# Kernel optimization log

Measured on AMD Instinct MI355X. Metric: run time of the kernel, lower is better.

## Reference

```python
import jax, jax.numpy as jnp
from jax import lax
import numpy as np

MARKER_NUM = 50000
E = 256          # embed_dim
D = 512          # d_model
K = 16           # sample_size / neighbor_num
B = 128
S = 128
BETA = 0.1
MAX_TIME = 1000.0


def setup_inputs() -> dict:
    key = jax.random.key(0)
    ks = jax.random.split(key, 12)
    def lin(k, fan_in, shape):
        return (jax.random.normal(k, shape, jnp.float32) / np.sqrt(fan_in)).astype(jnp.float32)
    return {
        "marker_data": jax.random.randint(ks[0], (B, S), 0, MARKER_NUM),
        "time_data": jax.random.uniform(ks[1], (B, S), jnp.float32),
        "mask_data": jnp.ones((B, S), jnp.float32),
        "embedding": jax.random.normal(ks[2], (MARKER_NUM, E), jnp.float32) * 0.05,
        "neighbor_list": jax.random.randint(ks[3], (MARKER_NUM, K), 0, MARKER_NUM),
        "neighbor_prob": jax.random.uniform(ks[4], (MARKER_NUM, K), jnp.float32),
        "W_te": lin(ks[5], 1, (1, E)), "b_te": jnp.zeros((E,), jnp.float32),
        "W_el": lin(ks[6], E, (E, D)), "b_el": jnp.zeros((D,), jnp.float32),
        "W_ih": lin(ks[7], D, (D, D)), "b_ih": jnp.zeros((D,), jnp.float32),
        "W_hh": lin(ks[8], D, (D, D)), "b_hh": jnp.zeros((D,), jnp.float32),
        "W_time": lin(ks[9], D, (D, 1)), "b_time": jnp.zeros((1,), jnp.float32),
        "W_mk": lin(ks[10], E + D, (E + D, 1)), "b_mk": jnp.zeros((1,), jnp.float32),
    }


def reference(marker_data, time_data, mask_data, embedding, neighbor_list, neighbor_prob,
              W_te, b_te, W_el, b_el, W_ih, b_ih, W_hh, b_hh, W_time, b_time, W_mk, b_mk):
    leaky = lambda x: jnp.where(x >= 0, x, 0.01 * x)  # LeakyReLU(0.01)
    Bn, Sn = marker_data.shape
    L = 1 + (Sn - 1) * (K - 1)  # final candidate_list / prob_list width
    R = 1 + (Sn - 1) * K        # final neighbor_prob_record width

    cand0 = jnp.zeros((Bn, L), jnp.int32).at[:, 0].set(marker_data[:, 0].astype(jnp.int32))
    prob0 = jnp.zeros((Bn, L), jnp.float32).at[:, 0].set(1.0)  # zero pad -> never sampled
    nrec0 = jnp.ones((Bn, R), jnp.float32)
    chosen0 = jnp.zeros((Bn, 1), jnp.int32)
    h0 = jnp.zeros((Bn, D), jnp.float32)
    carry0 = (h0, time_data[:, 0:1], marker_data[:, 0:1].astype(jnp.int32), cand0, prob0, nrec0, chosen0)
    keys = jax.random.split(jax.random.key(42), Sn - 1)

    def step(carry, xt):
        t, key = xt
        h, last_t, last_m, cand, prob, nrec, chosen = carry
        # embedding of (marker, time)
        time_emb = last_t @ W_te + b_te                       # (B,E)
        vec = embedding[last_m[:, 0]] + BETA * time_emb       # (B,E)
        x = leaky(vec @ W_el + b_el)                          # (B,D)
        # single-layer tanh RNN step (nn.RNN)
        h = jnp.tanh(x @ W_ih + b_ih + h @ W_hh + b_hh)
        new_t = last_t + jax.nn.softplus(h @ W_time + b_time)  # (B,1)
        new_mask = (new_t < MAX_TIME).astype(jnp.float32)
        # sampled neighbors of last marker
        neigh = neighbor_list[last_m[:, 0]].astype(jnp.int32)  # (B,K)
        p_neigh = neighbor_prob[last_m[:, 0]]                  # (B,K)
        nrec = lax.dynamic_update_slice(nrec, p_neigh, (0, 1 + t * K))
        inf = jnp.concatenate([embedding[neigh], jnp.broadcast_to(h[:, None, :], (Bn, K, D))], axis=-1)
        mprob = jax.nn.softmax((inf @ W_mk + b_mk)[..., 0], axis=1)  # (B,K)
        cand = lax.dynamic_update_slice(cand, neigh[:, 1:], (0, 1 + t * (K - 1)))
        chosen_p = jnp.take_along_axis(prob, chosen, 1)        # (B,1)
        attached = chosen_p * mprob                            # (B,K)
        prob = prob.at[jnp.arange(Bn), chosen[:, 0]].set(attached[:, 0])
        prob = lax.dynamic_update_slice(prob, attached[:, 1:], (0, 1 + t * (K - 1)))
        # torch.multinomial(prob_list, 1) == categorical over normalized probs
        logits = jnp.where(prob > 0, jnp.log(jnp.maximum(prob, 1e-38)), -1e30)
        new_chosen = jax.random.categorical(key, lax.stop_gradient(logits), axis=1)[:, None].astype(jnp.int32)
        new_m = jnp.take_along_axis(cand, new_chosen, 1)       # (B,1)
        sel_np = jnp.take_along_axis(nrec, new_chosen, 1)
        sel_sp = jnp.take_along_axis(prob, new_chosen, 1)
        new_carry = (h, new_t, new_m, cand, prob, nrec, new_chosen)
        return new_carry, (new_m[:, 0], new_t[:, 0], new_mask[:, 0], sel_np[:, 0], sel_sp[:, 0])

    _, (ms, ts, mk, nps, sps) = lax.scan(step, carry0, (jnp.arange(Sn - 1), keys))
    ones = jnp.ones((Bn, 1), jnp.float32)
    marker_res = jnp.concatenate([marker_data[:, 0:1].astype(jnp.int32), ms.T], axis=1)
    time_res = jnp.concatenate([time_data[:, 0:1], ts.T], axis=1)
    mask_res = jnp.concatenate([mask_data[:, 0:1], mk.T], axis=1)
    total_neighbor_prob = jnp.concatenate([ones, nps.T], axis=1)
    total_sample_prob = jnp.concatenate([ones, sps.T], axis=1)
    return (marker_res, time_res, mask_res, total_neighbor_prob, total_sample_prob)
```

## Files before the change

### kernel.cpp

```cpp
#include <hip/hip_runtime.h>
#include <stdint.h>
#include <stddef.h>

#define BB 128
#define SS 128
#define EE 256
#define DD 512
#define KK 16
#define LL 1906
#define RR 2033
#define NSTEP 127

static __device__ __forceinline__ uint32_t rotl32(uint32_t v, int r) {
  return (v << r) | (v >> (32 - r));
}

static __device__ __forceinline__ void tf2x32(uint32_t k0, uint32_t k1,
                                              uint32_t x0, uint32_t x1,
                                              uint32_t &o0, uint32_t &o1) {
  uint32_t ks2 = k0 ^ k1 ^ 0x1BD11BDAu;
  x0 += k0; x1 += k1;
#define TFR(r) { x0 += x1; x1 = rotl32(x1, (r)); x1 ^= x0; }
  TFR(13) TFR(15) TFR(26) TFR(6)
  x0 += k1;  x1 += ks2 + 1u;
  TFR(17) TFR(29) TFR(16) TFR(24)
  x0 += ks2; x1 += k0 + 2u;
  TFR(13) TFR(15) TFR(26) TFR(6)
  x0 += k0;  x1 += k1 + 3u;
  TFR(17) TFR(29) TFR(16) TFR(24)
  x0 += k1;  x1 += ks2 + 4u;
  TFR(13) TFR(15) TFR(26) TFR(6)
  x0 += ks2; x1 += k0 + 5u;
#undef TFR
  o0 = x0; o1 = x1;
}

static __device__ __forceinline__ float jax_gumbel(uint32_t bits) {
  float f = __uint_as_float((bits >> 9) | 0x3F800000u) - 1.0f;
  float u = fmaxf(f, 1.17549435e-38f);
  return -logf(-logf(u));
}

__global__ __launch_bounds__(1024, 4) void rnn_gen_kernel(
    const int*   __restrict__ marker_data,
    const float* __restrict__ time_data,
    const float* __restrict__ mask_data,
    const float* __restrict__ embedding,
    const int*   __restrict__ neighbor_list,
    const float* __restrict__ neighbor_prob,
    const float* __restrict__ W_te,
    const float* __restrict__ b_te,
    const float* __restrict__ W_el,
    const float* __restrict__ b_el,
    const float* __restrict__ W_ih,
    const float* __restrict__ b_ih,
    const float* __restrict__ W_hh,
    const float* __restrict__ b_hh,
    const float* __restrict__ W_time,
    const float* __restrict__ b_time,
    const float* __restrict__ W_mk,
    const float* __restrict__ b_mk,
    float* __restrict__ out)
{
  __shared__ double s_pd[8][DD];
  __shared__ double s_pd2[8][DD];
  __shared__ double s_edot[KK];
  __shared__ double s_rt[8];
  __shared__ double s_rm[8];
  __shared__ float  s_prob[LL];
  __shared__ int    s_cand[LL];
  __shared__ float  s_nrec[RR];
  __shared__ float  s_x[DD];
  __shared__ float  s_h[DD];
  __shared__ float  s_vec[EE];
  __shared__ float  s_red_z[16];
  __shared__ int    s_red_i[16];
  __shared__ int    s_neigh[KK];
  __shared__ float  s_last_t;
  __shared__ int    s_last_m;
  __shared__ int    s_chosen;
  __shared__ float  s_newt;
  __shared__ uint32_t s_k0, s_k1;

  const int b   = blockIdx.x;
  const int tid = threadIdx.x;

  for (int i = tid; i < LL; i += 1024) { s_prob[i] = 0.0f; s_cand[i] = 0; }
  for (int i = tid; i < RR; i += 1024) s_nrec[i] = 1.0f;
  if (tid < DD) s_h[tid] = 0.0f;
  if (tid == 0) {
    int   m0 = marker_data[b * SS];
    float t0 = time_data[b * SS];
    s_cand[0] = m0; s_prob[0] = 1.0f;
    s_last_m = m0; s_last_t = t0; s_chosen = 0;
    out[0 * BB * SS + b * SS + 0] = (float)m0;
    out[1 * BB * SS + b * SS + 0] = t0;
    out[2 * BB * SS + b * SS + 0] = mask_data[b * SS];
    out[3 * BB * SS + b * SS + 0] = 1.0f;
    out[4 * BB * SS + b * SS + 0] = 1.0f;
  }
  __syncthreads();

  for (int t = 0; t < NSTEP; ++t) {
    const int   m  = s_last_m;
    const float lt = s_last_t;

    if (tid == 768) {
      uint32_t o0, o1;
      tf2x32(0u, 42u, 0u, (uint32_t)t, o0, o1);
      s_k0 = o0; s_k1 = o1;
    }
    if (tid < EE) {
      float te = __fadd_rn(__fmul_rn(lt, W_te[tid]), b_te[tid]);
      s_vec[tid] = __fadd_rn(embedding[(size_t)m * EE + tid], __fmul_rn(0.1f, te));
    }
    if (tid >= 256 && tid < 256 + KK) {
      int k = tid - 256;
      int nb = neighbor_list[(size_t)m * KK + k];
      s_neigh[k] = nb;
      s_nrec[1 + t * KK + k] = neighbor_prob[(size_t)m * KK + k];
      if (k >= 1) s_cand[1 + t * (KK - 1) + (k - 1)] = nb;
    }
    __syncthreads();

    float4 ev0 = make_float4(0.f,0.f,0.f,0.f), ev1 = ev0;
    if (tid >= 512) {
      int k = (tid - 512) >> 5, l32 = tid & 31;
      const float4* er = (const float4*)(embedding + (size_t)s_neigh[k] * EE);
      ev0 = er[2 * l32]; ev1 = er[2 * l32 + 1];
    }
    const int jg = tid & 127;
    const int sl = tid >> 7;
    {
      const int i0 = sl << 5;
      const float4* W4 = (const float4*)W_el + (size_t)i0 * 128 + jg;
      double d0 = 0.0, d1 = 0.0, d2 = 0.0, d3 = 0.0;
#pragma unroll 4
      for (int i = 0; i < 32; i += 4) {
        float4 a4 = *(const float4*)&s_vec[i0 + i];
        float4 w0 = W4[0], w1 = W4[128], w2 = W4[256], w3 = W4[384];
        W4 += 512;
        d0 = fma((double)a4.x, (double)w0.x, d0); d1 = fma((double)a4.x, (double)w0.y, d1);
        d2 = fma((double)a4.x, (double)w0.z, d2); d3 = fma((double)a4.x, (double)w0.w, d3);
        d0 = fma((double)a4.y, (double)w1.x, d0); d1 = fma((double)a4.y, (double)w1.y, d1);
        d2 = fma((double)a4.y, (double)w1.z, d2); d3 = fma((double)a4.y, (double)w1.w, d3);
        d0 = fma((double)a4.z, (double)w2.x, d0); d1 = fma((double)a4.z, (double)w2.y, d1);
        d2 = fma((double)a4.z, (double)w2.z, d2); d3 = fma((double)a4.z, (double)w2.w, d3);
        d0 = fma((double)a4.w, (double)w3.x, d0); d1 = fma((double)a4.w, (double)w3.y, d1);
        d2 = fma((double)a4.w, (double)w3.z, d2); d3 = fma((double)a4.w, (double)w3.w, d3);
      }
      double* pd = &s_pd[sl][4 * jg];
      pd[0] = d0; pd[1] = d1; pd[2] = d2; pd[3] = d3;
    }
    {
      const int i0 = sl << 6;
      const float4* W4 = (const float4*)W_hh + (size_t)i0 * 128 + jg;
      double d0 = 0.0, d1 = 0.0, d2 = 0.0, d3 = 0.0;
#pragma unroll 4
      for (int i = 0; i < 64; i += 4) {
        float4 a4 = *(const float4*)&s_h[i0 + i];
        float4 w0 = W4[0], w1 = W4[128], w2 = W4[256], w3 = W4[384];
        W4 += 512;
        d0 = fma((double)a4.x, (double)w0.x, d0); d1 = fma((double)a4.x, (double)w0.y, d1);
        d2 = fma((double)a4.x, (double)w0.z, d2); d3 = fma((double)a4.x, (double)w0.w, d3);
        d0 = fma((double)a4.y, (double)w1.x, d0); d1 = fma((double)a4.y, (double)w1.y, d1);
        d2 = fma((double)a4.y, (double)w1.z, d2); d3 = fma((double)a4.y, (double)w1.w, d3);
        d0 = fma((double)a4.z, (double)w2.x, d0); d1 = fma((double)a4.z, (double)w2.y, d1);
        d2 = fma((double)a4.z, (double)w2.z, d2); d3 = fma((double)a4.z, (double)w2.w, d3);
        d0 = fma((double)a4.w, (double)w3.x, d0); d1 = fma((double)a4.w, (double)w3.y, d1);
        d2 = fma((double)a4.w, (double)w3.z, d2); d3 = fma((double)a4.w, (double)w3.w, d3);
      }
      double* pd = &s_pd2[sl][4 * jg];
      pd[0] = d0; pd[1] = d1; pd[2] = d2; pd[3] = d3;
    }
    __syncthreads();

    if (tid < DD) {
      double d = ((s_pd[0][tid] + s_pd[1][tid]) + (s_pd[2][tid] + s_pd[3][tid]))
               + ((s_pd[4][tid] + s_pd[5][tid]) + (s_pd[6][tid] + s_pd[7][tid]));
      float z = __fadd_rn((float)d, b_el[tid]);
      s_x[tid] = (z >= 0.0f) ? z : __fmul_rn(0.01f, z);
    }
    __syncthreads();

    {
      const int i0 = sl << 6;
      const float4* W4 = (const float4*)W_ih + (size_t)i0 * 128 + jg;
      double d0 = 0.0, d1 = 0.0, d2 = 0.0, d3 = 0.0;
#pragma unroll 4
      for (int i = 0; i < 64; i += 4) {
        float4 a4 = *(const float4*)&s_x[i0 + i];
        float4 w0 = W4[0], w1 = W4[128], w2 = W4[256], w3 = W4[384];
        W4 += 512;
        d0 = fma((double)a4.x, (double)w0.x, d0); d1 = fma((double)a4.x, (double)w0.y, d1);
        d2 = fma((double)a4.x, (double)w0.z, d2); d3 = fma((double)a4.x, (double)w0.w, d3);
        d0 = fma((double)a4.y, (double)w1.x, d0); d1 = fma((double)a4.y, (double)w1.y, d1);
        d2 = fma((double)a4.y, (double)w1.z, d2); d3 = fma((double)a4.y, (double)w1.w, d3);
        d0 = fma((double)a4.z, (double)w2.x, d0); d1 = fma((double)a4.z, (double)w2.y, d1);
        d2 = fma((double)a4.z, (double)w2.z, d2); d3 = fma((double)a4.z, (double)w2.w, d3);
        d0 = fma((double)a4.w, (double)w3.x, d0); d1 = fma((double)a4.w, (double)w3.y, d1);
        d2 = fma((double)a4.w, (double)w3.z, d2); d3 = fma((double)a4.w, (double)w3.w, d3);
      }
      double* pd = &s_pd[sl][4 * jg];
      pd[0] = d0; pd[1] = d1; pd[2] = d2; pd[3] = d3;
    }
    __syncthreads();

    if (tid < DD) {
      double ih = ((s_pd[0][tid] + s_pd[1][tid]) + (s_pd[2][tid] + s_pd[3][tid]))
                + ((s_pd[4][tid] + s_pd[5][tid]) + (s_pd[6][tid] + s_pd[7][tid]));
      double hh = ((s_pd2[0][tid] + s_pd2[1][tid]) + (s_pd2[2][tid] + s_pd2[3][tid]))
                + ((s_pd2[4][tid] + s_pd2[5][tid]) + (s_pd2[6][tid] + s_pd2[7][tid]));
      float p = __fadd_rn(__fadd_rn(__fadd_rn((float)ih, b_ih[tid]), (float)hh), b_hh[tid]);
      float hf = (float)tanh((double)p);
      s_h[tid] = hf;
      double hv = (double)hf;
      double pt = hv * (double)W_time[tid];
      double pm = hv * (double)W_mk[EE + tid];
      for (int off = 32; off > 0; off >>= 1) {
        pt += __shfl_down(pt, off);
        pm += __shfl_down(pm, off);
      }
      if ((tid & 63) == 0) { s_rt[tid >> 6] = pt; s_rm[tid >> 6] = pm; }
    } else {
      int k = (tid - 512) >> 5, l32 = tid & 31;
      const float4* wm4 = (const float4*)W_mk;
      float4 wm0 = wm4[2 * l32], wm1 = wm4[2 * l32 + 1];
      double acc = 0.0;
      acc = fma((double)ev0.x, (double)wm0.x, acc);
      acc = fma((double)ev0.y, (double)wm0.y, acc);
      acc = fma((double)ev0.z, (double)wm0.z, acc);
      acc = fma((double)ev0.w, (double)wm0.w, acc);
      acc = fma((double)ev1.x, (double)wm1.x, acc);
      acc = fma((double)ev1.y, (double)wm1.y, acc);
      acc = fma((double)ev1.z, (double)wm1.z, acc);
      acc = fma((double)ev1.w, (double)wm1.w, acc);
      for (int off = 16; off > 0; off >>= 1) acc += __shfl_down(acc, off, 32);
      if (l32 == 0) s_edot[k] = acc;
    }
    __syncthreads();

    if (tid < KK) {
      double hmk = ((s_rm[0] + s_rm[1]) + (s_rm[2] + s_rm[3]))
                 + ((s_rm[4] + s_rm[5]) + (s_rm[6] + s_rm[7]));
      float sc = __fadd_rn((float)(s_edot[tid] + hmk), b_mk[0]);
      float mx = sc;
      for (int k = 0; k < KK; ++k) mx = fmaxf(mx, __shfl(sc, k));
      float ee = expf(__fsub_rn(sc, mx));
      float ssum = 0.0f;
      for (int k = 0; k < KK; ++k) ssum = __fadd_rn(ssum, __shfl(ee, k));
      float cp = s_prob[s_chosen];
      float at = __fmul_rn(cp, __fdiv_rn(ee, ssum));
      if (tid == 0) s_prob[s_chosen] = at;
      else          s_prob[1 + t * (KK - 1) + (tid - 1)] = at;
    } else if (tid == 16) {
      double ht = ((s_rt[0] + s_rt[1]) + (s_rt[2] + s_rt[3]))
                + ((s_rt[4] + s_rt[5]) + (s_rt[6] + s_rt[7]));
      float td = __fadd_rn((float)ht, b_time[0]);
      float sp = __fadd_rn(fmaxf(td, 0.0f), log1pf(expf(-fabsf(td))));
      s_newt = __fadd_rn(s_last_t, sp);
    }
    __syncthreads();

    const int active = 16 + 15 * t;
    const uint32_t kk0 = s_k0, kk1 = s_k1;
    float bz = -3.0e38f;
    int   bi = 0x7FFFFFFF;
    for (int l = tid; l < active; l += 1024) {
      uint32_t i = (uint32_t)(b * LL + l);
      uint32_t o0, o1;
      tf2x32(kk0, kk1, 0u, i, o0, o1);
      float g  = jax_gumbel(o0 ^ o1);
      float pr = s_prob[l];
      float z  = (pr > 0.0f) ? __fadd_rn(logf(fmaxf(pr, 1e-38f)), g)
                             : __fadd_rn(-1e30f, g);
      if (z > bz) { bz = z; bi = l; }
    }
    for (int off = 32; off > 0; off >>= 1) {
      float oz = __shfl_down(bz, off);
      int   oi = __shfl_down(bi, off);
      if (oz > bz || (oz == bz && oi < bi)) { bz = oz; bi = oi; }
    }
    if ((tid & 63) == 0) { s_red_z[tid >> 6] = bz; s_red_i[tid >> 6] = bi; }
    __syncthreads();

    if (tid == 0) {
      float z0 = s_red_z[0]; int i0 = s_red_i[0];
      for (int w = 1; w < 16; ++w) {
        if (s_red_z[w] > z0 || (s_red_z[w] == z0 && s_red_i[w] < i0)) {
          z0 = s_red_z[w]; i0 = s_red_i[w];
        }
      }
      int   nm  = s_cand[i0];
      float np_ = s_nrec[i0];
      float sp_ = s_prob[i0];
      float nt  = s_newt;
      out[0 * BB * SS + b * SS + (t + 1)] = (float)nm;
      out[1 * BB * SS + b * SS + (t + 1)] = nt;
      out[2 * BB * SS + b * SS + (t + 1)] = (nt < 1000.0f) ? 1.0f : 0.0f;
      out[3 * BB * SS + b * SS + (t + 1)] = np_;
      out[4 * BB * SS + b * SS + (t + 1)] = sp_;
      s_chosen = i0; s_last_m = nm; s_last_t = nt;
    }
    __syncthreads();
  }
}

extern "C" void kernel_launch(void* const* d_in, const int* in_sizes, int n_in,
                              void* d_out, int out_size, void* d_ws, size_t ws_size,
                              hipStream_t stream) {
  (void)in_sizes; (void)n_in; (void)out_size; (void)d_ws; (void)ws_size;
  const int*   marker_data   = (const int*)  d_in[0];
  const float* time_data     = (const float*)d_in[1];
  const float* mask_data     = (const float*)d_in[2];
  const float* embedding     = (const float*)d_in[3];
  const int*   neighbor_list = (const int*)  d_in[4];
  const float* neighbor_prob = (const float*)d_in[5];
  const float* W_te   = (const float*)d_in[6];
  const float* b_te   = (const float*)d_in[7];
  const float* W_el   = (const float*)d_in[8];
  const float* b_el   = (const float*)d_in[9];
  const float* W_ih   = (const float*)d_in[10];
  const float* b_ih   = (const float*)d_in[11];
  const float* W_hh   = (const float*)d_in[12];
  const float* b_hh   = (const float*)d_in[13];
  const float* W_time = (const float*)d_in[14];
  const float* b_time = (const float*)d_in[15];
  const float* W_mk   = (const float*)d_in[16];
  const float* b_mk   = (const float*)d_in[17];
  float* out = (float*)d_out;

  hipLaunchKernelGGL(rnn_gen_kernel, dim3(BB), dim3(1024), 0, stream,
                     marker_data, time_data, mask_data, embedding,
                     neighbor_list, neighbor_prob,
                     W_te, b_te, W_el, b_el, W_ih, b_ih, W_hh, b_hh,
                     W_time, b_time, W_mk, b_mk, out);
}
```

Before: 3.713 ms.

## Split each batch row across two cooperating blocks with global-memory flag sync

Each sequence row is now handled by a pair of workgroups. Each block computes half of the output columns of the W_el, W_ih and W_hh matvecs, and the halves of x and h are swapped through a workspace using release/acquire flags and spin-waits. Block A alone does the sampling and publishes the chosen marker and time to block B. The W_hh matvec is moved to the start of the step so it can run before the marker handoff. This doubles the number of CUs working on the serial recurrence and halves per-block weight traffic, at the cost of cross-block spin synchronisation latency at several points per step, and it assumes all 256 blocks are co-resident.

```diff
diff --git a/kernel.cpp b/kernel.cpp
--- a/kernel.cpp
+++ b/kernel.cpp
@@ -10,6 +10,21 @@
 #define LL 1906
 #define RR 2033
 #define NSTEP 127
+
+#define WS_ROW_STRIDE 2048
+
+#define AT_ST(p, v)     __hip_atomic_store((p), (v), __ATOMIC_RELAXED, __HIP_MEMORY_SCOPE_AGENT)
+#define AT_LD(p)        __hip_atomic_load((p), __ATOMIC_RELAXED, __HIP_MEMORY_SCOPE_AGENT)
+#define AT_ST_REL(p, v) __hip_atomic_store((p), (v), __ATOMIC_RELEASE, __HIP_MEMORY_SCOPE_AGENT)
+#define AT_LD_ACQ(p)    __hip_atomic_load((p), __ATOMIC_ACQUIRE, __HIP_MEMORY_SCOPE_AGENT)
+
+static __device__ __forceinline__ void spin_ge(uint32_t* f, uint32_t want) {
+  int guard = 0;
+  while (AT_LD_ACQ(f) < want) {
+    __builtin_amdgcn_s_sleep(2);
+    if (++guard > (1 << 22)) break;
+  }
+}
 
 static __device__ __forceinline__ uint32_t rotl32(uint32_t v, int r) {
   return (v << r) | (v >> (32 - r));
@@ -41,38 +56,47 @@
   return -logf(-logf(u));
 }
 
-__global__ __launch_bounds__(1024, 4) void rnn_gen_kernel(
+#define FMA16(a4, w0, w1, w2, w3)                                              \
+  d0 = fma((double)a4.x, (double)w0.x, d0); d1 = fma((double)a4.x, (double)w0.y, d1); \
+  d2 = fma((double)a4.x, (double)w0.z, d2); d3 = fma((double)a4.x, (double)w0.w, d3); \
+  d0 = fma((double)a4.y, (double)w1.x, d0); d1 = fma((double)a4.y, (double)w1.y, d1); \
+  d2 = fma((double)a4.y, (double)w1.z, d2); d3 = fma((double)a4.y, (double)w1.w, d3); \
+  d0 = fma((double)a4.z, (double)w2.x, d0); d1 = fma((double)a4.z, (double)w2.y, d1); \
+  d2 = fma((double)a4.z, (double)w2.z, d2); d3 = fma((double)a4.z, (double)w2.w, d3); \
+  d0 = fma((double)a4.w, (double)w3.x, d0); d1 = fma((double)a4.w, (double)w3.y, d1); \
+  d2 = fma((double)a4.w, (double)w3.z, d2); d3 = fma((double)a4.w, (double)w3.w, d3);
+
+__global__ void init_flags_kernel(uint32_t* ws) {
+  if (threadIdx.x < 5) ws[(size_t)blockIdx.x * WS_ROW_STRIDE + threadIdx.x * 32] = 0u;
+}
+
+__global__ __launch_bounds__(1024, 4) void rnn_pair_kernel(
     const int*   __restrict__ marker_data,
     const float* __restrict__ time_data,
     const float* __restrict__ mask_data,
     const float* __restrict__ embedding,
     const int*   __restrict__ neighbor_list,
     const float* __restrict__ neighbor_prob,
-    const float* __restrict__ W_te,
-    const float* __restrict__ b_te,
-    const float* __restrict__ W_el,
-    const float* __restrict__ b_el,
-    const float* __restrict__ W_ih,
-    const float* __restrict__ b_ih,
-    const float* __restrict__ W_hh,
-    const float* __restrict__ b_hh,
-    const float* __restrict__ W_time,
-    const float* __restrict__ b_time,
-    const float* __restrict__ W_mk,
-    const float* __restrict__ b_mk,
+    const float* __restrict__ W_te, const float* __restrict__ b_te,
+    const float* __restrict__ W_el, const float* __restrict__ b_el,
+    const float* __restrict__ W_ih, const float* __restrict__ b_ih,
+    const float* __restrict__ W_hh, const float* __restrict__ b_hh,
+    const float* __restrict__ W_time, const float* __restrict__ b_time,
+    const float* __restrict__ W_mk, const float* __restrict__ b_mk,
+    float* __restrict__ ws,
     float* __restrict__ out)
 {
-  __shared__ double s_pd[8][DD];
-  __shared__ double s_pd2[8][DD];
-  __shared__ double s_edot[KK];
-  __shared__ double s_rt[8];
-  __shared__ double s_rm[8];
+  __shared__ double s_pd[16][256];
+  __shared__ double s_pd2[16][256];
   __shared__ float  s_prob[LL];
   __shared__ int    s_cand[LL];
   __shared__ float  s_nrec[RR];
   __shared__ float  s_x[DD];
   __shared__ float  s_h[DD];
   __shared__ float  s_vec[EE];
+  __shared__ double s_edot[KK];
+  __shared__ double s_rt[8];
+  __shared__ double s_rm[8];
   __shared__ float  s_red_z[16];
   __shared__ int    s_red_i[16];
   __shared__ int    s_neigh[KK];
@@ -82,234 +106,279 @@
   __shared__ float  s_newt;
   __shared__ uint32_t s_k0, s_k1;
 
-  const int b   = blockIdx.x;
-  const int tid = threadIdx.x;
-
-  for (int i = tid; i < LL; i += 1024) { s_prob[i] = 0.0f; s_cand[i] = 0; }
-  for (int i = tid; i < RR; i += 1024) s_nrec[i] = 1.0f;
+  const int  bid  = blockIdx.x;
+  const bool isA  = (bid < BB);
+  const int  row  = isA ? bid : bid - BB;
+  const int  tid  = threadIdx.x;
+  const int  own0 = isA ? 0 : 256;
+  const int  oq   = own0 >> 2;
+
+  float*    wrow   = ws + (size_t)row * WS_ROW_STRIDE;
+  uint32_t* urow   = (uint32_t*)wrow;
+  uint32_t* fx_own = urow + (isA ? 0 : 32);
+  uint32_t* fx_oth = urow + (isA ? 32 : 0);
+  uint32_t* fh_own = urow + (isA ? 64 : 96);
+  uint32_t* fh_oth = urow + (isA ? 96 : 64);
+  uint32_t* fm     = urow + 128;
+  uint32_t* pay_m  = urow + 160;
+  float*    pay_t  = wrow + 161;
+  float*    x_own  = wrow + (isA ? 256 : 512);
+  float*    x_oth  = wrow + (isA ? 512 : 256);
+  float*    h_own  = wrow + (isA ? 768 : 1024);
+  float*    h_oth  = wrow + (isA ? 1024 : 768);
+
+  if (isA) {
+    for (int i = tid; i < LL; i += 1024) { s_prob[i] = 0.0f; s_cand[i] = 0; }
+    for (int i = tid; i < RR; i += 1024) s_nrec[i] = 1.0f;
+  }
   if (tid < DD) s_h[tid] = 0.0f;
   if (tid == 0) {
-    int   m0 = marker_data[b * SS];
-    float t0 = time_data[b * SS];
-    s_cand[0] = m0; s_prob[0] = 1.0f;
+    int   m0 = marker_data[row * SS];
+    float t0 = time_data[row * SS];
     s_last_m = m0; s_last_t = t0; s_chosen = 0;
-    out[0 * BB * SS + b * SS + 0] = (float)m0;
-    out[1 * BB * SS + b * SS + 0] = t0;
-    out[2 * BB * SS + b * SS + 0] = mask_data[b * SS];
-    out[3 * BB * SS + b * SS + 0] = 1.0f;
-    out[4 * BB * SS + b * SS + 0] = 1.0f;
+    if (isA) {
+      s_cand[0] = m0; s_prob[0] = 1.0f;
+      out[0 * BB * SS + row * SS + 0] = (float)m0;
+      out[1 * BB * SS + row * SS + 0] = t0;
+      out[2 * BB * SS + row * SS + 0] = mask_data[row * SS];
+      out[3 * BB * SS + row * SS + 0] = 1.0f;
+      out[4 * BB * SS + row * SS + 0] = 1.0f;
+    }
   }
   __syncthreads();
 
+  const int jg = tid & 63;
+  const int sl = tid >> 6;
+
   for (int t = 0; t < NSTEP; ++t) {
+    {
+      const int i0 = sl << 5;
+      const float4* W4 = (const float4*)W_hh + (size_t)i0 * 128 + oq + jg;
+      double d0 = 0.0, d1 = 0.0, d2 = 0.0, d3 = 0.0;
+#pragma unroll 4
+      for (int i = 0; i < 32; i += 4) {
+        float4 a4 = *(const float4*)&s_h[i0 + i];
+        float4 w0 = W4[0], w1 = W4[128], w2 = W4[256], w3 = W4[384];
+        W4 += 512;
+        FMA16(a4, w0, w1, w2, w3)
+      }
+      double* pd = &s_pd2[sl][4 * jg];
+      pd[0] = d0; pd[1] = d1; pd[2] = d2; pd[3] = d3;
+    }
+
+    if (!isA && t > 0 && tid == 0) {
+      spin_ge(fm, (uint32_t)t);
+      s_last_m = (int)AT_LD(pay_m);
+      s_last_t = AT_LD(pay_t);
+    }
+    __syncthreads();
     const int   m  = s_last_m;
     const float lt = s_last_t;
 
-    if (tid == 768) {
-      uint32_t o0, o1;
-      tf2x32(0u, 42u, 0u, (uint32_t)t, o0, o1);
-      s_k0 = o0; s_k1 = o1;
-    }
     if (tid < EE) {
       float te = __fadd_rn(__fmul_rn(lt, W_te[tid]), b_te[tid]);
       s_vec[tid] = __fadd_rn(embedding[(size_t)m * EE + tid], __fmul_rn(0.1f, te));
     }
-    if (tid >= 256 && tid < 256 + KK) {
-      int k = tid - 256;
-      int nb = neighbor_list[(size_t)m * KK + k];
-      s_neigh[k] = nb;
-      s_nrec[1 + t * KK + k] = neighbor_prob[(size_t)m * KK + k];
-      if (k >= 1) s_cand[1 + t * (KK - 1) + (k - 1)] = nb;
-    }
-    __syncthreads();
-
-    float4 ev0 = make_float4(0.f,0.f,0.f,0.f), ev1 = ev0;
-    if (tid >= 512) {
+    if (isA) {
+      if (tid == 768) {
+        uint32_t o0, o1;
+        tf2x32(0u, 42u, 0u, (uint32_t)t, o0, o1);
+        s_k0 = o0; s_k1 = o1;
+      }
+      if (tid >= 256 && tid < 256 + KK) {
+        int k = tid - 256;
+        int nb = neighbor_list[(size_t)m * KK + k];
+        s_neigh[k] = nb;
+        s_nrec[1 + t * KK + k] = neighbor_prob[(size_t)m * KK + k];
+        if (k >= 1) s_cand[1 + t * (KK - 1) + (k - 1)] = nb;
+      }
+    }
+    __syncthreads();
+
+    float4 ev0 = make_float4(0.f, 0.f, 0.f, 0.f), ev1 = ev0;
+    if (isA && tid >= 512) {
       int k = (tid - 512) >> 5, l32 = tid & 31;
       const float4* er = (const float4*)(embedding + (size_t)s_neigh[k] * EE);
       ev0 = er[2 * l32]; ev1 = er[2 * l32 + 1];
     }
-    const int jg = tid & 127;
-    const int sl = tid >> 7;
+    {
+      const int i0 = sl << 4;
+      const float4* W4 = (const float4*)W_el + (size_t)i0 * 128 + oq + jg;
+      double d0 = 0.0, d1 = 0.0, d2 = 0.0, d3 = 0.0;
+#pragma unroll 4
+      for (int i = 0; i < 16; i += 4) {
+        float4 a4 = *(const float4*)&s_vec[i0 + i];
+        float4 w0 = W4[0], w1 = W4[128], w2 = W4[256], w3 = W4[384];
+        W4 += 512;
+        FMA16(a4, w0, w1, w2, w3)
+      }
+      double* pd = &s_pd[sl][4 * jg];
+      pd[0] = d0; pd[1] = d1; pd[2] = d2; pd[3] = d3;
+    }
+    __syncthreads();
+
+    if (tid < 256) {
+      double d = (((s_pd[0][tid] + s_pd[1][tid]) + (s_pd[2][tid] + s_pd[3][tid]))
+                + ((s_pd[4][tid] + s_pd[5][tid]) + (s_pd[6][tid] + s_pd[7][tid])))
+               + (((s_pd[8][tid] + s_pd[9][tid]) + (s_pd[10][tid] + s_pd[11][tid]))
+                + ((s_pd[12][tid] + s_pd[13][tid]) + (s_pd[14][tid] + s_pd[15][tid])));
+      float z = __fadd_rn((float)d, b_el[own0 + tid]);
+      float xv = (z >= 0.0f) ? z : __fmul_rn(0.01f, z);
+      s_x[own0 + tid] = xv;
+      AT_ST(&x_own[tid], xv);
+    }
+    __syncthreads();
+    if (tid == 0) {
+      AT_ST_REL(fx_own, (uint32_t)(t + 1));
+      spin_ge(fx_oth, (uint32_t)(t + 1));
+    }
+    __syncthreads();
+    if (tid < 256) s_x[(own0 ^ 256) + tid] = AT_LD(&x_oth[tid]);
+    __syncthreads();
+
     {
       const int i0 = sl << 5;
-      const float4* W4 = (const float4*)W_el + (size_t)i0 * 128 + jg;
+      const float4* W4 = (const float4*)W_ih + (size_t)i0 * 128 + oq + jg;
       double d0 = 0.0, d1 = 0.0, d2 = 0.0, d3 = 0.0;
 #pragma unroll 4
       for (int i = 0; i < 32; i += 4) {
-        float4 a4 = *(const float4*)&s_vec[i0 + i];
-        float4 w0 = W4[0], w1 = W4[128], w2 = W4[256], w3 = W4[384];
-        W4 += 512;
-        d0 = fma((double)a4.x, (double)w0.x, d0); d1 = fma((double)a4.x, (double)w0.y, d1);
-        d2 = fma((double)a4.x, (double)w0.z, d2); d3 = fma((double)a4.x, (double)w0.w, d3);
-        d0 = fma((double)a4.y, (double)w1.x, d0); d1 = fma((double)a4.y, (double)w1.y, d1);
-        d2 = fma((double)a4.y, (double)w1.z, d2); d3 = fma((double)a4.y, (double)w1.w, d3);
-        d0 = fma((double)a4.z, (double)w2.x, d0); d1 = fma((double)a4.z, (double)w2.y, d1);
-        d2 = fma((double)a4.z, (double)w2.z, d2); d3 = fma((double)a4.z, (double)w2.w, d3);
-        d0 = fma((double)a4.w, (double)w3.x, d0); d1 = fma((double)a4.w, (double)w3.y, d1);
-        d2 = fma((double)a4.w, (double)w3.z, d2); d3 = fma((double)a4.w, (double)w3.w, d3);
-      }
-      double* pd = &s_pd[sl][4 * jg];
-      pd[0] = d0; pd[1] = d1; pd[2] = d2; pd[3] = d3;
-    }
-    {
-      const int i0 = sl << 6;
-      const float4* W4 = (const float4*)W_hh + (size_t)i0 * 128 + jg;
-      double d0 = 0.0, d1 = 0.0, d2 = 0.0, d3 = 0.0;
-#pragma unroll 4
-      for (int i = 0; i < 64; i += 4) {
-        float4 a4 = *(const float4*)&s_h[i0 + i];
-        float4 w0 = W4[0], w1 = W4[128], w2 = W4[256], w3 = W4[384];
-        W4 += 512;
-        d0 = fma((double)a4.x, (double)w0.x, d0); d1 = fma((double)a4.x, (double)w0.y, d1);
-        d2 = fma((double)a4.x, (double)w0.z, d2); d3 = fma((double)a4.x, (double)w0.w, d3);
-        d0 = fma((double)a4.y, (double)w1.x, d0); d1 = fma((double)a4.y, (double)w1.y, d1);
-        d2 = fma((double)a4.y, (double)w1.z, d2); d3 = fma((double)a4.y, (double)w1.w, d3);
-        d0 = fma((double)a4.z, (double)w2.x, d0); d1 = fma((double)a4.z, (double)w2.y, d1);
-        d2 = fma((double)a4.z, (double)w2.z, d2); d3 = fma((double)a4.z, (double)w2.w, d3);
-        d0 = fma((double)a4.w, (double)w3.x, d0); d1 = fma((double)a4.w, (double)w3.y, d1);
-        d2 = fma((double)a4.w, (double)w3.z, d2); d3 = fma((double)a4.w, (double)w3.w, d3);
-      }
-      double* pd = &s_pd2[sl][4 * jg];
-      pd[0] = d0; pd[1] = d1; pd[2] = d2; pd[3] = d3;
-    }
-    __syncthreads();
-
-    if (tid < DD) {
-      double d = ((s_pd[0][tid] + s_pd[1][tid]) + (s_pd[2][tid] + s_pd[3][tid]))
-               + ((s_pd[4][tid] + s_pd[5][tid]) + (s_pd[6][tid] + s_pd[7][tid]));
-      float z = __fadd_rn((float)d, b_el[tid]);
-      s_x[tid] = (z >= 0.0f) ? z : __fmul_rn(0.01f, z);
-    }
-    __syncthreads();
-
-    {
-      const int i0 = sl << 6;
-      const float4* W4 = (const float4*)W_ih + (size_t)i0 * 128 + jg;
-      double d0 = 0.0, d1 = 0.0, d2 = 0.0, d3 = 0.0;
-#pragma unroll 4
-      for (int i = 0; i < 64; i += 4) {
         float4 a4 = *(const float4*)&s_x[i0 + i];
         float4 w0 = W4[0], w1 = W4[128], w2 = W4[256], w3 = W4[384];
         W4 += 512;
-        d0 = fma((double)a4.x, (double)w0.x, d0); d1 = fma((double)a4.x, (double)w0.y, d1);
-        d2 = fma((double)a4.x, (double)w0.z, d2); d3 = fma((double)a4.x, (double)w0.w, d3);
-        d0 = fma((double)a4.y, (double)w1.x, d0); d1 = fma((double)a4.y, (double)w1.y, d1);
-        d2 = fma((double)a4.y, (double)w1.z, d2); d3 = fma((double)a4.y, (double)w1.w, d3);
-        d0 = fma((double)a4.z, (double)w2.x, d0); d1 = fma((double)a4.z, (double)w2.y, d1);
-        d2 = fma((double)a4.z, (double)w2.z, d2); d3 = fma((double)a4.z, (double)w2.w, d3);
-        d0 = fma((double)a4.w, (double)w3.x, d0); d1 = fma((double)a4.w, (double)w3.y, d1);
-        d2 = fma((double)a4.w, (double)w3.z, d2); d3 = fma((double)a4.w, (double)w3.w, d3);
+        FMA16(a4, w0, w1, w2, w3)
       }
       double* pd = &s_pd[sl][4 * jg];
       pd[0] = d0; pd[1] = d1; pd[2] = d2; pd[3] = d3;
     }
     __syncthreads();
 
-    if (tid < DD) {
-      double ih = ((s_pd[0][tid] + s_pd[1][tid]) + (s_pd[2][tid] + s_pd[3][tid]))
-                + ((s_pd[4][tid] + s_pd[5][tid]) + (s_pd[6][tid] + s_pd[7][tid]));
-      double hh = ((s_pd2[0][tid] + s_pd2[1][tid]) + (s_pd2[2][tid] + s_pd2[3][tid]))
-                + ((s_pd2[4][tid] + s_pd2[5][tid]) + (s_pd2[6][tid] + s_pd2[7][tid]));
-      float p = __fadd_rn(__fadd_rn(__fadd_rn((float)ih, b_ih[tid]), (float)hh), b_hh[tid]);
+    if (tid < 256) {
+      int j = own0 + tid;
+      double ih = (((s_pd[0][tid] + s_pd[1][tid]) + (s_pd[2][tid] + s_pd[3][tid]))
+                 + ((s_pd[4][tid] + s_pd[5][tid]) + (s_pd[6][tid] + s_pd[7][tid])))
+                + (((s_pd[8][tid] + s_pd[9][tid]) + (s_pd[10][tid] + s_pd[11][tid]))
+                 + ((s_pd[12][tid] + s_pd[13][tid]) + (s_pd[14][tid] + s_pd[15][tid])));
+      double hh = (((s_pd2[0][tid] + s_pd2[1][tid]) + (s_pd2[2][tid] + s_pd2[3][tid]))
+                 + ((s_pd2[4][tid] + s_pd2[5][tid]) + (s_pd2[6][tid] + s_pd2[7][tid])))
+                + (((s_pd2[8][tid] + s_pd2[9][tid]) + (s_pd2[10][tid] + s_pd2[11][tid]))
+                 + ((s_pd2[12][tid] + s_pd2[13][tid]) + (s_pd2[14][tid] + s_pd2[15][tid])));
+      float p = __fadd_rn(__fadd_rn(__fadd_rn((float)ih, b_ih[j]), (float)hh), b_hh[j]);
       float hf = (float)tanh((double)p);
-      s_h[tid] = hf;
-      double hv = (double)hf;
-      double pt = hv * (double)W_time[tid];
-      double pm = hv * (double)W_mk[EE + tid];
+      s_h[j] = hf;
+      AT_ST(&h_own[tid], hf);
+    }
+    __syncthreads();
+    if (tid == 0) {
+      AT_ST_REL(fh_own, (uint32_t)(t + 1));
+      spin_ge(fh_oth, (uint32_t)(t + 1));
+    }
+    __syncthreads();
+    if (tid < 256) s_h[(own0 ^ 256) + tid] = AT_LD(&h_oth[tid]);
+    __syncthreads();
+
+    if (isA) {
+      if (tid < DD) {
+        double hv = (double)s_h[tid];
+        double pt = hv * (double)W_time[tid];
+        double pm = hv * (double)W_mk[EE + tid];
+        for (int off = 32; off > 0; off >>= 1) {
+          pt += __shfl_down(pt, off);
+          pm += __shfl_down(pm, off);
+        }
+        if ((tid & 63) == 0) { s_rt[tid >> 6] = pt; s_rm[tid >> 6] = pm; }
+      } else {
+        int l32 = tid & 31;
+        const float4* wm4 = (const float4*)W_mk;
+        float4 wm0 = wm4[2 * l32], wm1 = wm4[2 * l32 + 1];
+        double acc = 0.0;
+        acc = fma((double)ev0.x, (double)wm0.x, acc);
+        acc = fma((double)ev0.y, (double)wm0.y, acc);
+        acc = fma((double)ev0.z, (double)wm0.z, acc);
+        acc = fma((double)ev0.w, (double)wm0.w, acc);
+        acc = fma((double)ev1.x, (double)wm1.x, acc);
+        acc = fma((double)ev1.y, (double)wm1.y, acc);
+        acc = fma((double)ev1.z, (double)wm1.z, acc);
+        acc = fma((double)ev1.w, (double)wm1.w, acc);
+        for (int off = 16; off > 0; off >>= 1) acc += __shfl_down(acc, off, 32);
+        if (l32 == 0) s_edot[(tid - 512) >> 5] = acc;
+      }
+      __syncthreads();
+
+      if (tid < KK) {
+        double hmk = ((s_rm[0] + s_rm[1]) + (s_rm[2] + s_rm[3]))
+                   + ((s_rm[4] + s_rm[5]) + (s_rm[6] + s_rm[7]));
+        float sc = __fadd_rn((float)(s_edot[tid] + hmk), b_mk[0]);
+        float mx = sc;
+        for (int k = 0; k < KK; ++k) mx = fmaxf(mx, __shfl(sc, k));
+        float ee = expf(__fsub_rn(sc, mx));
+        float ssum = 0.0f;
+        for (int k = 0; k < KK; ++k) ssum = __fadd_rn(ssum, __shfl(ee, k));
+        float cp = s_prob[s_chosen];
+        float at = __fmul_rn(cp, __fdiv_rn(ee, ssum));
+        if (tid == 0) s_prob[s_chosen] = at;
+        else          s_prob[1 + t * (KK - 1) + (tid - 1)] = at;
+      } else if (tid == 16) {
+        double ht = ((s_rt[0] + s_rt[1]) + (s_rt[2] + s_rt[3]))
+                  + ((s_rt[4] + s_rt[5]) + (s_rt[6] + s_rt[7]));
+        float td = __fadd_rn((float)ht, b_time[0]);
+        float sp = __fadd_rn(fmaxf(td, 0.0f), log1pf(expf(-fabsf(td))));
+        s_newt = __fadd_rn(s_last_t, sp);
+      }
+      __syncthreads();
+
+      const int active = 16 + 15 * t;
+      const uint32_t kk0 = s_k0, kk1 = s_k1;
+      float bz = -3.0e38f;
+      int   bi = 0x7FFFFFFF;
+      for (int l = tid; l < active; l += 1024) {
+        uint32_t i = (uint32_t)(row * LL + l);
+        uint32_t o0, o1;
+        tf2x32(kk0, kk1, 0u, i, o0, o1);
+        float g  = jax_gumbel(o0 ^ o1);
+        float pr = s_prob[l];
+        float z  = (pr > 0.0f) ? __fadd_rn(logf(fmaxf(pr, 1e-38f)), g)
+                               : __fadd_rn(-1e30f, g);
+        if (z > bz) { bz = z; bi = l; }
+      }
       for (int off = 32; off > 0; off >>= 1) {
-        pt += __shfl_down(pt, off);
-        pm += __shfl_down(pm, off);
-      }
-      if ((tid & 63) == 0) { s_rt[tid >> 6] = pt; s_rm[tid >> 6] = pm; }
-    } else {
-      int k = (tid - 512) >> 5, l32 = tid & 31;
-      const float4* wm4 = (const float4*)W_mk;
-      float4 wm0 = wm4[2 * l32], wm1 = wm4[2 * l32 + 1];
-      double acc = 0.0;
-      acc = fma((double)ev0.x, (double)wm0.x, acc);
-      acc = fma((double)ev0.y, (double)wm0.y, acc);
-      acc = fma((double)ev0.z, (double)wm0.z, acc);
-      acc = fma((double)ev0.w, (double)wm0.w, acc);
-      acc = fma((double)ev1.x, (double)wm1.x, acc);
-      acc = fma((double)ev1.y, (double)wm1.y, acc);
-      acc = fma((double)ev1.z, (double)wm1.z, acc);
-      acc = fma((double)ev1.w, (double)wm1.w, acc);
-      for (int off = 16; off > 0; off >>= 1) acc += __shfl_down(acc, off, 32);
-      if (l32 == 0) s_edot[k] = acc;
-    }
-    __syncthreads();
-
-    if (tid < KK) {
-      double hmk = ((s_rm[0] + s_rm[1]) + (s_rm[2] + s_rm[3]))
-                 + ((s_rm[4] + s_rm[5]) + (s_rm[6] + s_rm[7]));
-      float sc = __fadd_rn((float)(s_edot[tid] + hmk), b_mk[0]);
-      float mx = sc;
-      for (int k = 0; k < KK; ++k) mx = fmaxf(mx, __shfl(sc, k));
-      float ee = expf(__fsub_rn(sc, mx));
-      float ssum = 0.0f;
-      for (int k = 0; k < KK; ++k) ssum = __fadd_rn(ssum, __shfl(ee, k));
-      float cp = s_prob[s_chosen];
-      float at = __fmul_rn(cp, __fdiv_rn(ee, ssum));
-      if (tid == 0) s_prob[s_chosen] = at;
-      else          s_prob[1 + t * (KK - 1) + (tid - 1)] = at;
-    } else if (tid == 16) {
-      double ht = ((s_rt[0] + s_rt[1]) + (s_rt[2] + s_rt[3]))
-                + ((s_rt[4] + s_rt[5]) + (s_rt[6] + s_rt[7]));
-      float td = __fadd_rn((float)ht, b_time[0]);
-      float sp = __fadd_rn(fmaxf(td, 0.0f), log1pf(expf(-fabsf(td))));
-      s_newt = __fadd_rn(s_last_t, sp);
-    }
-    __syncthreads();
-
-    const int active = 16 + 15 * t;
-    const uint32_t kk0 = s_k0, kk1 = s_k1;
-    float bz = -3.0e38f;
-    int   bi = 0x7FFFFFFF;
-    for (int l = tid; l < active; l += 1024) {
-      uint32_t i = (uint32_t)(b * LL + l);
-      uint32_t o0, o1;
-      tf2x32(kk0, kk1, 0u, i, o0, o1);
-      float g  = jax_gumbel(o0 ^ o1);
-      float pr = s_prob[l];
-      float z  = (pr > 0.0f) ? __fadd_rn(logf(fmaxf(pr, 1e-38f)), g)
-                             : __fadd_rn(-1e30f, g);
-      if (z > bz) { bz = z; bi = l; }
-    }
-    for (int off = 32; off > 0; off >>= 1) {
-      float oz = __shfl_down(bz, off);
-      int   oi = __shfl_down(bi, off);
-      if (oz > bz || (oz == bz && oi < bi)) { bz = oz; bi = oi; }
-    }
-    if ((tid & 63) == 0) { s_red_z[tid >> 6] = bz; s_red_i[tid >> 6] = bi; }
-    __syncthreads();
-
-    if (tid == 0) {
-      float z0 = s_red_z[0]; int i0 = s_red_i[0];
-      for (int w = 1; w < 16; ++w) {
-        if (s_red_z[w] > z0 || (s_red_z[w] == z0 && s_red_i[w] < i0)) {
-          z0 = s_red_z[w]; i0 = s_red_i[w];
+        float oz = __shfl_down(bz, off);
+        int   oi = __shfl_down(bi, off);
+        if (oz > bz || (oz == bz && oi < bi)) { bz = oz; bi = oi; }
+      }
+      if ((tid & 63) == 0) { s_red_z[tid >> 6] = bz; s_red_i[tid >> 6] = bi; }
+      __syncthreads();
+
+      if (tid == 0) {
+        float z0 = s_red_z[0]; int i0 = s_red_i[0];
+        for (int w = 1; w < 16; ++w) {
+          if (s_red_z[w] > z0 || (s_red_z[w] == z0 && s_red_i[w] < i0)) {
+            z0 = s_red_z[w]; i0 = s_red_i[w];
+          }
         }
-      }
-      int   nm  = s_cand[i0];
-      float np_ = s_nrec[i0];
-      float sp_ = s_prob[i0];
-      float nt  = s_newt;
-      out[0 * BB * SS + b * SS + (t + 1)] = (float)nm;
-      out[1 * BB * SS + b * SS + (t + 1)] = nt;
-      out[2 * BB * SS + b * SS + (t + 1)] = (nt < 1000.0f) ? 1.0f : 0.0f;
-      out[3 * BB * SS + b * SS + (t + 1)] = np_;
-      out[4 * BB * SS + b * SS + (t + 1)] = sp_;
-      s_chosen = i0; s_last_m = nm; s_last_t = nt;
-    }
-    __syncthreads();
+        int   nm  = s_cand[i0];
+        float np_ = s_nrec[i0];
+        float sp_ = s_prob[i0];
+        float nt  = s_newt;
+        out[0 * BB * SS + row * SS + (t + 1)] = (float)nm;
+        out[1 * BB * SS + row * SS + (t + 1)] = nt;
+        out[2 * BB * SS + row * SS + (t + 1)] = (nt < 1000.0f) ? 1.0f : 0.0f;
+        out[3 * BB * SS + row * SS + (t + 1)] = np_;
+        out[4 * BB * SS + row * SS + (t + 1)] = sp_;
+        s_chosen = i0; s_last_m = nm; s_last_t = nt;
+        AT_ST(pay_m, (uint32_t)nm);
+        AT_ST(pay_t, nt);
+        AT_ST_REL(fm, (uint32_t)(t + 1));
+      }
+      __syncthreads();
+    }
   }
 }
 
 extern "C" void kernel_launch(void* const* d_in, const int* in_sizes, int n_in,
                               void* d_out, int out_size, void* d_ws, size_t ws_size,
                               hipStream_t stream) {
-  (void)in_sizes; (void)n_in; (void)out_size; (void)d_ws; (void)ws_size;
+  (void)in_sizes; (void)n_in; (void)out_size;
+  if (ws_size < (size_t)BB * WS_ROW_STRIDE * 4) return;
   const int*   marker_data   = (const int*)  d_in[0];
   const float* time_data     = (const float*)d_in[1];
   const float* mask_data     = (const float*)d_in[2];
@@ -329,10 +398,12 @@
   const float* W_mk   = (const float*)d_in[16];
   const float* b_mk   = (const float*)d_in[17];
   float* out = (float*)d_out;
-
-  hipLaunchKernelGGL(rnn_gen_kernel, dim3(BB), dim3(1024), 0, stream,
+  float* ws  = (float*)d_ws;
+
+  hipLaunchKernelGGL(init_flags_kernel, dim3(BB), dim3(64), 0, stream, (uint32_t*)d_ws);
+  hipLaunchKernelGGL(rnn_pair_kernel, dim3(2 * BB), dim3(1024), 0, stream,
                      marker_data, time_data, mask_data, embedding,
                      neighbor_list, neighbor_prob,
                      W_te, b_te, W_el, b_el, W_ih, b_ih, W_hh, b_hh,
-                     W_time, b_time, W_mk, b_mk, out);
-}
+                     W_time, b_time, W_mk, b_mk, ws, out);
+}
```

Measured after the change: 8.652 ms. 133% more time.
